# Performance work log

Measured on AMD Instinct MI355X. Metric: run time of the kernel, lower is better.

## Reference

```python
import jax, jax.numpy as jnp
import numpy as np

B, N, M, E = 2, 16384, 16384, 49152
W_CHAMFER, W_EDGE = 1.0, 0.1


def setup_inputs() -> dict:
    key = jax.random.key(0)
    k1, k2, k3 = jax.random.split(key, 3)
    pred_verts = jax.random.normal(k1, (B, N, 3), dtype=jnp.float32)
    target_verts = jax.random.normal(k2, (B, M, 3), dtype=jnp.float32)
    edges = jax.random.randint(k3, (E, 2), 0, N, dtype=jnp.int64)
    return {"pred_verts": pred_verts, "target_verts": target_verts, "edges": edges}


def reference(pred_verts, target_verts, edges):
    # --- Chamfer distance (torch.cdist + bidirectional min) ---
    # Squared-distance expansion avoids materializing the B x N x M x 3 diff tensor.
    p2 = jnp.sum(pred_verts * pred_verts, axis=-1)            # [B, N]
    t2 = jnp.sum(target_verts * target_verts, axis=-1)        # [B, M]
    cross = jnp.einsum('bnd,bmd->bnm', pred_verts, target_verts)  # [B, N, M]
    d2 = p2[:, :, None] + t2[:, None, :] - 2.0 * cross
    dist = jnp.sqrt(jnp.maximum(d2, 0.0))                     # [B, N, M]
    c_loss = jnp.mean(jnp.min(dist, axis=2)) + jnp.mean(jnp.min(dist, axis=1))

    # --- Edge-length variance regularization (vectorized over batch) ---
    v1 = pred_verts[:, edges[:, 0]]                           # [B, E, 3]
    v2 = pred_verts[:, edges[:, 1]]                           # [B, E, 3]
    edge_lengths = jnp.linalg.norm(v1 - v2, axis=-1)          # [B, E]
    # torch.var defaults to unbiased (ddof=1); mean over batch == sum/B
    e_loss = jnp.mean(jnp.var(edge_lengths, axis=1, ddof=1))

    total_loss = W_CHAMFER * c_loss + W_EDGE * e_loss
    return (total_loss, c_loss, e_loss)
```

## Files before the change

kernel.cpp:

```cpp
#include <hip/hip_runtime.h>
#include <float.h>

#define B_SZ 2
#define N_SZ 16384
#define E_SZ 49152

#define TPB 512
#define WAVES (TPB / 64)
#define ROWS_PER_BLOCK 128
#define CHUNK 1024
#define NCHUNK (N_SZ / CHUNK)
#define TILES_PER_CHUNK (CHUNK / 32)
#define TILES_PER_CG (TILES_PER_CHUNK / 4)

#define CH_BLOCKS_PER_DIR (B_SZ * N_SZ / ROWS_PER_BLOCK)
#define CH_BLOCKS (2 * CH_BLOCKS_PER_DIR)
#define EDGE_BLOCKS (B_SZ * E_SZ / TPB)

#define PLANE_BYTES (N_SZ * 16)
#define BATCH_FRAG_BYTES (2 * PLANE_BYTES)
#define DIR_FRAG_BYTES (B_SZ * BATCH_FRAG_BYTES)
#define SUMS_OFF (2 * DIR_FRAG_BYTES)

typedef short short8 __attribute__((ext_vector_type(8)));
typedef float f32x16 __attribute__((ext_vector_type(16)));

__device__ inline short f2bf(float f) {
    unsigned u = __float_as_uint(f);
    unsigned r = (u + 0x7fffu + ((u >> 16) & 1u)) >> 16;
    return (short)r;
}
__device__ inline float bf2f(short s) {
    return __uint_as_float(((unsigned)(unsigned short)s) << 16);
}

typedef __attribute__((address_space(1))) const unsigned int g_u32;
typedef __attribute__((address_space(3))) unsigned int l_u32;
__device__ inline void gload_lds16(const void* g, void* l) {
    __builtin_amdgcn_global_load_lds((g_u32*)g, (l_u32*)l, 16, 0, 0);
}

__global__ __launch_bounds__(TPB) void prep(const float* __restrict__ pred,
                                            const float* __restrict__ tgt,
                                            char* __restrict__ ws) {
    int idx = blockIdx.x * TPB + threadIdx.x;
    double* sums = (double*)(ws + SUMS_OFF);
    if (blockIdx.x == 0 && threadIdx.x < 6) sums[threadIdx.x] = 0.0;

    const bool isTgt = idx < B_SZ * N_SZ;
    int row = isTgt ? idx : idx - B_SZ * N_SZ;
    int batch = row >> 14, pt = row & (N_SZ - 1);
    const float* src = (isTgt ? tgt : pred) + (size_t)row * 3;
    char* base = ws + (isTgt ? 0 : DIR_FRAG_BYTES) + (size_t)batch * BATCH_FRAG_BYTES;

    float tx = src[0], ty = src[1], tz = src[2];
    short hx = f2bf(tx), hy = f2bf(ty), hz = f2bf(tz);
    short lx = f2bf(tx - bf2f(hx)), ly = f2bf(ty - bf2f(hy)), lz = f2bf(tz - bf2f(hz));
    float t2 = fmaf(tx, tx, fmaf(ty, ty, tz * tz));
    short t2h = f2bf(t2), t2l = f2bf(t2 - bf2f(t2h));
    const short one = 0x3f80;

    *(short8*)(base + (size_t)pt * 16) = (short8){hx, hy, hz, hx, hy, hz, one, one};
    *(short8*)(base + PLANE_BYTES + (size_t)pt * 16) =
        (short8){lx, ly, lz, t2h, t2l, 0, 0, 0};
}

__global__ __launch_bounds__(TPB, 4) void main_kernel(
    const float* __restrict__ pred, const float* __restrict__ tgt,
    const int* __restrict__ edges, char* __restrict__ ws)
{
    __shared__ __align__(16) char sB[2][2 * CHUNK * 16];
    __shared__ float wred[WAVES], wred2[WAVES];
    __shared__ int rowMin[ROWS_PER_BLOCK];
    double* sums = (double*)(ws + SUMS_OFF);
    const int lane = threadIdx.x & 63;
    const int wv = threadIdx.x >> 6;
    const int t = threadIdx.x;

    if (blockIdx.x < CH_BLOCKS) {
        const int dir = blockIdx.x >> 8;
        const int xb = blockIdx.x & 255;
        const int batch = xb >> 7;
        const int rowInB = (xb & 127) * ROWS_PER_BLOCK;
        const float* P = dir ? tgt : pred;
        const char* fragBase = ws + (size_t)dir * DIR_FRAG_BYTES
                                  + (size_t)batch * BATCH_FRAG_BYTES;
        const int bl = lane & 31;
        const int half = lane >> 5;
        const int rp = wv & 1;
        const int cg = wv >> 1;

        auto stage = [&](int c, int buf) {
            const char* p0 = fragBase + (size_t)c * (CHUNK * 16);
            const char* p1 = fragBase + PLANE_BYTES + (size_t)c * (CHUNK * 16);
            char* d = sB[buf];
            gload_lds16(p0 + (size_t)t * 16,         d + (size_t)t * 16);
            gload_lds16(p0 + (size_t)(t + TPB) * 16, d + (size_t)(t + TPB) * 16);
            gload_lds16(p1 + (size_t)t * 16,         d + (size_t)(t + 2 * TPB) * 16);
            gload_lds16(p1 + (size_t)(t + TPB) * 16, d + (size_t)(t + 3 * TPB) * 16);
        };
        stage(0, 0);
        if (t < ROWS_PER_BLOCK) rowMin[t] = 0x7f7fffff;

        const short one = 0x3f80;
        short8 af[2];
        #pragma unroll
        for (int j = 0; j < 2; j++) {
            int r = batch * N_SZ + rowInB + rp * 64 + j * 32 + bl;
            const float* p = P + (size_t)r * 3;
            float px = p[0], py = p[1], pz = p[2];
            float ax = -2.f * px, ay = -2.f * py, az = -2.f * pz;
            short ahx = f2bf(ax), ahy = f2bf(ay), ahz = f2bf(az);
            short alx = f2bf(ax - bf2f(ahx)), aly = f2bf(ay - bf2f(ahy)),
                  alz = f2bf(az - bf2f(ahz));
            float p2 = fmaf(px, px, fmaf(py, py, pz * pz));
            short p2h = f2bf(p2), p2l = f2bf(p2 - bf2f(p2h));
            af[j] = half == 0
                ? (short8){ahx, ahy, ahz, alx, aly, alz, p2h, p2l}
                : (short8){ahx, ahy, ahz, one, one, 0, 0, 0};
        }

        float acc0[16], acc1[16];
        #pragma unroll
        for (int e = 0; e < 16; e++) { acc0[e] = FLT_MAX; acc1[e] = FLT_MAX; }
        const f32x16 zc = {0.f, 0.f, 0.f, 0.f, 0.f, 0.f, 0.f, 0.f,
                           0.f, 0.f, 0.f, 0.f, 0.f, 0.f, 0.f, 0.f};

        __syncthreads();

        for (int c = 0; c < NCHUNK; c++) {
            int buf = c & 1;
            if (c + 1 < NCHUNK) stage(c + 1, buf ^ 1);
            const char* bp = sB[buf] + half * (CHUNK * 16)
                           + (size_t)(cg * TILES_PER_CG * 32 + bl) * 16;
            #pragma unroll 1
            for (int mt = 0; mt < TILES_PER_CG; mt += 2) {
                short8 b0 = *(const short8*)(bp + (mt * 32) * 16);
                short8 b1 = *(const short8*)(bp + (mt * 32 + 32) * 16);
                {
                    f32x16 r0 = __builtin_amdgcn_mfma_f32_32x32x16_bf16(af[0], b0, zc, 0, 0, 0);
                    f32x16 r1 = __builtin_amdgcn_mfma_f32_32x32x16_bf16(af[0], b1, zc, 0, 0, 0);
                    #pragma unroll
                    for (int e = 0; e < 16; e++)
                        acc0[e] = fminf(fminf(r0[e], r1[e]), acc0[e]);
                }
                {
                    f32x16 r0 = __builtin_amdgcn_mfma_f32_32x32x16_bf16(af[1], b0, zc, 0, 0, 0);
                    f32x16 r1 = __builtin_amdgcn_mfma_f32_32x32x16_bf16(af[1], b1, zc, 0, 0, 0);
                    #pragma unroll
                    for (int e = 0; e < 16; e++)
                        acc1[e] = fminf(fminf(r0[e], r1[e]), acc1[e]);
                }
            }
            __syncthreads();
        }

        #pragma unroll
        for (int j = 0; j < 2; j++) {
            #pragma unroll
            for (int e = 0; e < 16; e++) {
                float v = (j == 0) ? acc0[e] : acc1[e];
                v = fminf(v, __shfl_xor(v, 1));
                v = fminf(v, __shfl_xor(v, 2));
                v = fminf(v, __shfl_xor(v, 4));
                v = fminf(v, __shfl_xor(v, 8));
                v = fminf(v, __shfl_xor(v, 16));
                if (bl == 0) {
                    int row = rp * 64 + j * 32 + (e & 3) + 8 * (e >> 2) + 4 * half;
                    atomicMin(&rowMin[row], __float_as_int(fmaxf(v, 0.f)));
                }
            }
        }
        __syncthreads();

        if (t < ROWS_PER_BLOCK) {
            float s = sqrtf(__int_as_float(rowMin[t]));
            #pragma unroll
            for (int o = 32; o > 0; o >>= 1) s += __shfl_down(s, o, 64);
            if (lane == 0) wred[wv] = s;
        }
        __syncthreads();
        if (t == 0) atomicAdd(&sums[dir], (double)(wred[0] + wred[1]));
    } else {
        int idx = (blockIdx.x - CH_BLOCKS) * TPB + threadIdx.x;
        int b = idx >= E_SZ;
        int e = idx - b * E_SZ;
        int2 ee = ((const int2*)edges)[e];
        const float* p0 = pred + ((size_t)b * N_SZ + (size_t)ee.x) * 3;
        const float* p1 = pred + ((size_t)b * N_SZ + (size_t)ee.y) * 3;
        float dx = p0[0] - p1[0], dy = p0[1] - p1[1], dz = p0[2] - p1[2];
        float len = sqrtf(dx * dx + dy * dy + dz * dz);
        float s = len, q = len * len;
        for (int o = 32; o > 0; o >>= 1) {
            s += __shfl_down(s, o, 64);
            q += __shfl_down(q, o, 64);
        }
        if (lane == 0) { wred[wv] = s; wred2[wv] = q; }
        __syncthreads();
        if (threadIdx.x == 0) {
            float ts = 0.f, tq = 0.f;
            #pragma unroll
            for (int w = 0; w < WAVES; w++) { ts += wred[w]; tq += wred2[w]; }
            atomicAdd(&sums[2 + 2 * b], (double)ts);
            atomicAdd(&sums[3 + 2 * b], (double)tq);
        }
    }
}

__global__ void final_kernel(const char* __restrict__ ws, float* __restrict__ out) {
    const double* sums = (const double*)(ws + SUMS_OFF);
    double c = sums[0] / (double)(B_SZ * N_SZ) + sums[1] / (double)(B_SZ * N_SZ);
    double e = 0.0;
    #pragma unroll
    for (int b = 0; b < B_SZ; b++) {
        double s = sums[2 + 2 * b], q = sums[3 + 2 * b];
        e += (q - s * s / (double)E_SZ) / (double)(E_SZ - 1);
    }
    e *= (1.0 / B_SZ);
    double tot = 1.0 * c + 0.1 * e;
    out[0] = (float)tot;
    out[1] = (float)c;
    out[2] = (float)e;
}

extern "C" void kernel_launch(void* const* d_in, const int* in_sizes, int n_in,
                              void* d_out, int out_size, void* d_ws, size_t ws_size,
                              hipStream_t stream) {
    const float* pred = (const float*)d_in[0];
    const float* tgt  = (const float*)d_in[1];
    const int* edges  = (const int*)d_in[2];
    float* out = (float*)d_out;
    char* ws = (char*)d_ws;

    prep<<<dim3((2 * B_SZ * N_SZ) / TPB), TPB, 0, stream>>>(pred, tgt, ws);

    main_kernel<<<dim3(CH_BLOCKS + EDGE_BLOCKS), TPB, 0, stream>>>(
        pred, tgt, edges, ws);

    final_kernel<<<dim3(1), dim3(1), 0, stream>>>(ws, out);
}
```

Measured before the change: 103.5 us.

## Fuse prep, chamfer, edge and final stages into one cooperative kernel

Replaces three kernel launches with a single cooperative kernel of 256 blocks that runs prep, a grid sync, the edge and chamfer stages, another grid sync, and the final reduction. Each block now handles both chamfer directions in sequence instead of one block per direction. Edge sums go straight to global double atomics per wave instead of a block reduction, and the inner tile loop is fully unrolled. This removes launch gaps and the tail kernel, at the cost of grid-wide sync overhead, half as many resident blocks, more double atomics, and less parallelism for overlapping the chamfer work.

```diff
diff --git a/kernel.cpp b/kernel.cpp
--- a/kernel.cpp
+++ b/kernel.cpp
@@ -1,22 +1,23 @@
 #include <hip/hip_runtime.h>
+#include <hip/hip_cooperative_groups.h>
 #include <float.h>
+
+namespace cg = cooperative_groups;
 
 #define B_SZ 2
 #define N_SZ 16384
 #define E_SZ 49152
 
+#define GRID 256
 #define TPB 512
 #define WAVES (TPB / 64)
+#define REPS 2
 #define ROWS_PER_BLOCK 128
 #define CHUNK 1024
 #define NCHUNK (N_SZ / CHUNK)
 #define TILES_PER_CHUNK (CHUNK / 32)
 #define TILES_PER_CG (TILES_PER_CHUNK / 4)
 
-#define CH_BLOCKS_PER_DIR (B_SZ * N_SZ / ROWS_PER_BLOCK)
-#define CH_BLOCKS (2 * CH_BLOCKS_PER_DIR)
-#define EDGE_BLOCKS (B_SZ * E_SZ / TPB)
-
 #define PLANE_BYTES (N_SZ * 16)
 #define BATCH_FRAG_BYTES (2 * PLANE_BYTES)
 #define DIR_FRAG_BYTES (B_SZ * BATCH_FRAG_BYTES)
@@ -40,55 +41,75 @@
     __builtin_amdgcn_global_load_lds((g_u32*)g, (l_u32*)l, 16, 0, 0);
 }
 
-__global__ __launch_bounds__(TPB) void prep(const float* __restrict__ pred,
-                                            const float* __restrict__ tgt,
-                                            char* __restrict__ ws) {
-    int idx = blockIdx.x * TPB + threadIdx.x;
-    double* sums = (double*)(ws + SUMS_OFF);
-    if (blockIdx.x == 0 && threadIdx.x < 6) sums[threadIdx.x] = 0.0;
-
-    const bool isTgt = idx < B_SZ * N_SZ;
-    int row = isTgt ? idx : idx - B_SZ * N_SZ;
-    int batch = row >> 14, pt = row & (N_SZ - 1);
-    const float* src = (isTgt ? tgt : pred) + (size_t)row * 3;
-    char* base = ws + (isTgt ? 0 : DIR_FRAG_BYTES) + (size_t)batch * BATCH_FRAG_BYTES;
-
-    float tx = src[0], ty = src[1], tz = src[2];
-    short hx = f2bf(tx), hy = f2bf(ty), hz = f2bf(tz);
-    short lx = f2bf(tx - bf2f(hx)), ly = f2bf(ty - bf2f(hy)), lz = f2bf(tz - bf2f(hz));
-    float t2 = fmaf(tx, tx, fmaf(ty, ty, tz * tz));
-    short t2h = f2bf(t2), t2l = f2bf(t2 - bf2f(t2h));
-    const short one = 0x3f80;
-
-    *(short8*)(base + (size_t)pt * 16) = (short8){hx, hy, hz, hx, hy, hz, one, one};
-    *(short8*)(base + PLANE_BYTES + (size_t)pt * 16) =
-        (short8){lx, ly, lz, t2h, t2l, 0, 0, 0};
-}
-
-__global__ __launch_bounds__(TPB, 4) void main_kernel(
+__global__ __launch_bounds__(TPB, 2) void mega(
     const float* __restrict__ pred, const float* __restrict__ tgt,
-    const int* __restrict__ edges, char* __restrict__ ws)
+    const int* __restrict__ edges, char* __restrict__ ws,
+    float* __restrict__ out)
 {
     __shared__ __align__(16) char sB[2][2 * CHUNK * 16];
-    __shared__ float wred[WAVES], wred2[WAVES];
+    __shared__ float wred[WAVES];
     __shared__ int rowMin[ROWS_PER_BLOCK];
     double* sums = (double*)(ws + SUMS_OFF);
     const int lane = threadIdx.x & 63;
     const int wv = threadIdx.x >> 6;
     const int t = threadIdx.x;
-
-    if (blockIdx.x < CH_BLOCKS) {
-        const int dir = blockIdx.x >> 8;
-        const int xb = blockIdx.x & 255;
-        const int batch = xb >> 7;
-        const int rowInB = (xb & 127) * ROWS_PER_BLOCK;
+    const int gid = blockIdx.x * TPB + threadIdx.x;
+    cg::grid_group grid = cg::this_grid();
+
+    if (gid < 6) sums[gid] = 0.0;
+    if (gid < 2 * B_SZ * N_SZ) {
+        const bool isTgt = gid < B_SZ * N_SZ;
+        int row = isTgt ? gid : gid - B_SZ * N_SZ;
+        int batch = row >> 14, pt = row & (N_SZ - 1);
+        const float* src = (isTgt ? tgt : pred) + (size_t)row * 3;
+        char* base = ws + (isTgt ? 0 : DIR_FRAG_BYTES)
+                        + (size_t)batch * BATCH_FRAG_BYTES;
+        float tx = src[0], ty = src[1], tz = src[2];
+        short hx = f2bf(tx), hy = f2bf(ty), hz = f2bf(tz);
+        short lx = f2bf(tx - bf2f(hx)), ly = f2bf(ty - bf2f(hy)),
+              lz = f2bf(tz - bf2f(hz));
+        float t2 = fmaf(tx, tx, fmaf(ty, ty, tz * tz));
+        short t2h = f2bf(t2), t2l = f2bf(t2 - bf2f(t2h));
+        const short onep = 0x3f80;
+        *(short8*)(base + (size_t)pt * 16) =
+            (short8){hx, hy, hz, hx, hy, hz, onep, onep};
+        *(short8*)(base + PLANE_BYTES + (size_t)pt * 16) =
+            (short8){lx, ly, lz, t2h, t2l, 0, 0, 0};
+    }
+    grid.sync();
+
+    if (gid < 2 * E_SZ) {
+        int b = gid >= E_SZ;
+        int e = gid - b * E_SZ;
+        int2 ee = ((const int2*)edges)[e];
+        const float* p0 = pred + ((size_t)b * N_SZ + (size_t)ee.x) * 3;
+        const float* p1 = pred + ((size_t)b * N_SZ + (size_t)ee.y) * 3;
+        float dx = p0[0] - p1[0], dy = p0[1] - p1[1], dz = p0[2] - p1[2];
+        float len = sqrtf(dx * dx + dy * dy + dz * dz);
+        float s = len, q = len * len;
+        for (int o = 32; o > 0; o >>= 1) {
+            s += __shfl_down(s, o, 64);
+            q += __shfl_down(q, o, 64);
+        }
+        if (lane == 0) {
+            atomicAdd(&sums[2 + 2 * b], (double)s);
+            atomicAdd(&sums[3 + 2 * b], (double)q);
+        }
+    }
+
+    const int bl = lane & 31;
+    const int half = lane >> 5;
+    const int rp = wv & 1;
+    const int cg_ = wv >> 1;
+    const int batch = blockIdx.x >> 7;
+    const int rowInB = (blockIdx.x & 127) * ROWS_PER_BLOCK;
+    const short one = 0x3f80;
+
+    for (int rep = 0; rep < REPS; rep++) {
+        const int dir = rep;
         const float* P = dir ? tgt : pred;
         const char* fragBase = ws + (size_t)dir * DIR_FRAG_BYTES
                                   + (size_t)batch * BATCH_FRAG_BYTES;
-        const int bl = lane & 31;
-        const int half = lane >> 5;
-        const int rp = wv & 1;
-        const int cg = wv >> 1;
 
         auto stage = [&](int c, int buf) {
             const char* p0 = fragBase + (size_t)c * (CHUNK * 16);
@@ -102,7 +123,6 @@
         stage(0, 0);
         if (t < ROWS_PER_BLOCK) rowMin[t] = 0x7f7fffff;
 
-        const short one = 0x3f80;
         short8 af[2];
         #pragma unroll
         for (int j = 0; j < 2; j++) {
@@ -132,8 +152,8 @@
             int buf = c & 1;
             if (c + 1 < NCHUNK) stage(c + 1, buf ^ 1);
             const char* bp = sB[buf] + half * (CHUNK * 16)
-                           + (size_t)(cg * TILES_PER_CG * 32 + bl) * 16;
-            #pragma unroll 1
+                           + (size_t)(cg_ * TILES_PER_CG * 32 + bl) * 16;
+            #pragma unroll
             for (int mt = 0; mt < TILES_PER_CG; mt += 2) {
                 short8 b0 = *(const short8*)(bp + (mt * 32) * 16);
                 short8 b1 = *(const short8*)(bp + (mt * 32 + 32) * 16);
@@ -181,46 +201,23 @@
         }
         __syncthreads();
         if (t == 0) atomicAdd(&sums[dir], (double)(wred[0] + wred[1]));
-    } else {
-        int idx = (blockIdx.x - CH_BLOCKS) * TPB + threadIdx.x;
-        int b = idx >= E_SZ;
-        int e = idx - b * E_SZ;
-        int2 ee = ((const int2*)edges)[e];
-        const float* p0 = pred + ((size_t)b * N_SZ + (size_t)ee.x) * 3;
-        const float* p1 = pred + ((size_t)b * N_SZ + (size_t)ee.y) * 3;
-        float dx = p0[0] - p1[0], dy = p0[1] - p1[1], dz = p0[2] - p1[2];
-        float len = sqrtf(dx * dx + dy * dy + dz * dz);
-        float s = len, q = len * len;
-        for (int o = 32; o > 0; o >>= 1) {
-            s += __shfl_down(s, o, 64);
-            q += __shfl_down(q, o, 64);
-        }
-        if (lane == 0) { wred[wv] = s; wred2[wv] = q; }
-        __syncthreads();
-        if (threadIdx.x == 0) {
-            float ts = 0.f, tq = 0.f;
-            #pragma unroll
-            for (int w = 0; w < WAVES; w++) { ts += wred[w]; tq += wred2[w]; }
-            atomicAdd(&sums[2 + 2 * b], (double)ts);
-            atomicAdd(&sums[3 + 2 * b], (double)tq);
-        }
-    }
-}
-
-__global__ void final_kernel(const char* __restrict__ ws, float* __restrict__ out) {
-    const double* sums = (const double*)(ws + SUMS_OFF);
-    double c = sums[0] / (double)(B_SZ * N_SZ) + sums[1] / (double)(B_SZ * N_SZ);
-    double e = 0.0;
-    #pragma unroll
-    for (int b = 0; b < B_SZ; b++) {
-        double s = sums[2 + 2 * b], q = sums[3 + 2 * b];
-        e += (q - s * s / (double)E_SZ) / (double)(E_SZ - 1);
-    }
-    e *= (1.0 / B_SZ);
-    double tot = 1.0 * c + 0.1 * e;
-    out[0] = (float)tot;
-    out[1] = (float)c;
-    out[2] = (float)e;
+    }
+
+    grid.sync();
+    if (blockIdx.x == 0 && threadIdx.x == 0) {
+        double c = sums[0] / (double)(B_SZ * N_SZ) + sums[1] / (double)(B_SZ * N_SZ);
+        double e = 0.0;
+        #pragma unroll
+        for (int b = 0; b < B_SZ; b++) {
+            double s = sums[2 + 2 * b], q = sums[3 + 2 * b];
+            e += (q - s * s / (double)E_SZ) / (double)(E_SZ - 1);
+        }
+        e *= (1.0 / B_SZ);
+        double tot = 1.0 * c + 0.1 * e;
+        out[0] = (float)tot;
+        out[1] = (float)c;
+        out[2] = (float)e;
+    }
 }
 
 extern "C" void kernel_launch(void* const* d_in, const int* in_sizes, int n_in,
@@ -232,10 +229,6 @@
     float* out = (float*)d_out;
     char* ws = (char*)d_ws;
 
-    prep<<<dim3((2 * B_SZ * N_SZ) / TPB), TPB, 0, stream>>>(pred, tgt, ws);
-
-    main_kernel<<<dim3(CH_BLOCKS + EDGE_BLOCKS), TPB, 0, stream>>>(
-        pred, tgt, edges, ws);
-
-    final_kernel<<<dim3(1), dim3(1), 0, stream>>>(ws, out);
-}
+    void* args[] = {(void*)&pred, (void*)&tgt, (void*)&edges, (void*)&ws, (void*)&out};
+    hipLaunchCooperativeKernel((void*)mega, dim3(GRID), dim3(TPB), args, 0, stream);
+}
```

Result: slower. 244.6 us (+136.3%).

## Replace LDS double-buffered staging with direct global register prefetch of B fragments

Applied to the files above, without the earlier changes.

Removes the shared-memory chunk staging (global_load_lds double buffer plus per-chunk barriers) and has each wave load its B-operand fragments straight from global memory into registers, prefetching the next four tiles while the MFMAs run on the current ones. Each column group now walks a contiguous quarter of all tiles instead of a slice of each chunk. The launch-bounds occupancy hint drops from 4 to 2 blocks per CU to give more registers for the prefetched fragments. This removes LDS traffic and barrier stalls but relies on L2/L1 caching, since every block rereads the whole fragment array from global memory, and lower occupancy may expose latency.

```diff
diff --git a/kernel.cpp b/kernel.cpp
--- a/kernel.cpp
+++ b/kernel.cpp
@@ -8,10 +8,8 @@
 #define TPB 512
 #define WAVES (TPB / 64)
 #define ROWS_PER_BLOCK 128
-#define CHUNK 1024
-#define NCHUNK (N_SZ / CHUNK)
-#define TILES_PER_CHUNK (CHUNK / 32)
-#define TILES_PER_CG (TILES_PER_CHUNK / 4)
+#define NTILES (N_SZ / 32)
+#define TILES_PER_CG (NTILES / 4)
 
 #define CH_BLOCKS_PER_DIR (B_SZ * N_SZ / ROWS_PER_BLOCK)
 #define CH_BLOCKS (2 * CH_BLOCKS_PER_DIR)
@@ -32,12 +30,6 @@
 }
 __device__ inline float bf2f(short s) {
     return __uint_as_float(((unsigned)(unsigned short)s) << 16);
-}
-
-typedef __attribute__((address_space(1))) const unsigned int g_u32;
-typedef __attribute__((address_space(3))) unsigned int l_u32;
-__device__ inline void gload_lds16(const void* g, void* l) {
-    __builtin_amdgcn_global_load_lds((g_u32*)g, (l_u32*)l, 16, 0, 0);
 }
 
 __global__ __launch_bounds__(TPB) void prep(const float* __restrict__ pred,
@@ -65,11 +57,10 @@
         (short8){lx, ly, lz, t2h, t2l, 0, 0, 0};
 }
 
-__global__ __launch_bounds__(TPB, 4) void main_kernel(
+__global__ __launch_bounds__(TPB, 2) void main_kernel(
     const float* __restrict__ pred, const float* __restrict__ tgt,
     const int* __restrict__ edges, char* __restrict__ ws)
 {
-    __shared__ __align__(16) char sB[2][2 * CHUNK * 16];
     __shared__ float wred[WAVES], wred2[WAVES];
     __shared__ int rowMin[ROWS_PER_BLOCK];
     double* sums = (double*)(ws + SUMS_OFF);
@@ -90,16 +81,6 @@
         const int rp = wv & 1;
         const int cg = wv >> 1;
 
-        auto stage = [&](int c, int buf) {
-            const char* p0 = fragBase + (size_t)c * (CHUNK * 16);
-            const char* p1 = fragBase + PLANE_BYTES + (size_t)c * (CHUNK * 16);
-            char* d = sB[buf];
-            gload_lds16(p0 + (size_t)t * 16,         d + (size_t)t * 16);
-            gload_lds16(p0 + (size_t)(t + TPB) * 16, d + (size_t)(t + TPB) * 16);
-            gload_lds16(p1 + (size_t)t * 16,         d + (size_t)(t + 2 * TPB) * 16);
-            gload_lds16(p1 + (size_t)(t + TPB) * 16, d + (size_t)(t + 3 * TPB) * 16);
-        };
-        stage(0, 0);
         if (t < ROWS_PER_BLOCK) rowMin[t] = 0x7f7fffff;
 
         const short one = 0x3f80;
@@ -126,33 +107,44 @@
         const f32x16 zc = {0.f, 0.f, 0.f, 0.f, 0.f, 0.f, 0.f, 0.f,
                            0.f, 0.f, 0.f, 0.f, 0.f, 0.f, 0.f, 0.f};
 
-        __syncthreads();
-
-        for (int c = 0; c < NCHUNK; c++) {
-            int buf = c & 1;
-            if (c + 1 < NCHUNK) stage(c + 1, buf ^ 1);
-            const char* bp = sB[buf] + half * (CHUNK * 16)
-                           + (size_t)(cg * TILES_PER_CG * 32 + bl) * 16;
-            #pragma unroll 1
-            for (int mt = 0; mt < TILES_PER_CG; mt += 2) {
-                short8 b0 = *(const short8*)(bp + (mt * 32) * 16);
-                short8 b1 = *(const short8*)(bp + (mt * 32 + 32) * 16);
-                {
-                    f32x16 r0 = __builtin_amdgcn_mfma_f32_32x32x16_bf16(af[0], b0, zc, 0, 0, 0);
-                    f32x16 r1 = __builtin_amdgcn_mfma_f32_32x32x16_bf16(af[0], b1, zc, 0, 0, 0);
-                    #pragma unroll
-                    for (int e = 0; e < 16; e++)
-                        acc0[e] = fminf(fminf(r0[e], r1[e]), acc0[e]);
-                }
-                {
-                    f32x16 r0 = __builtin_amdgcn_mfma_f32_32x32x16_bf16(af[1], b0, zc, 0, 0, 0);
-                    f32x16 r1 = __builtin_amdgcn_mfma_f32_32x32x16_bf16(af[1], b1, zc, 0, 0, 0);
-                    #pragma unroll
-                    for (int e = 0; e < 16; e++)
-                        acc1[e] = fminf(fminf(r0[e], r1[e]), acc1[e]);
-                }
+        const char* bbase = fragBase + (size_t)half * PLANE_BYTES
+                                     + (size_t)bl * 16;
+        const int tbase = cg * TILES_PER_CG;
+        auto ldb = [&](int tc) {
+            return *(const short8*)(bbase + (size_t)tc * 512);
+        };
+
+        #define DOPAIR(X0, X1)                                                 \
+            do {                                                               \
+                f32x16 r0 = __builtin_amdgcn_mfma_f32_32x32x16_bf16(af[0], X0, zc, 0, 0, 0); \
+                f32x16 r1 = __builtin_amdgcn_mfma_f32_32x32x16_bf16(af[0], X1, zc, 0, 0, 0); \
+                _Pragma("unroll")                                              \
+                for (int e = 0; e < 16; e++)                                   \
+                    acc0[e] = fminf(fminf(r0[e], r1[e]), acc0[e]);             \
+                f32x16 s0 = __builtin_amdgcn_mfma_f32_32x32x16_bf16(af[1], X0, zc, 0, 0, 0); \
+                f32x16 s1 = __builtin_amdgcn_mfma_f32_32x32x16_bf16(af[1], X1, zc, 0, 0, 0); \
+                _Pragma("unroll")                                              \
+                for (int e = 0; e < 16; e++)                                   \
+                    acc1[e] = fminf(fminf(s0[e], s1[e]), acc1[e]);             \
+            } while (0)
+
+        short8 b0 = ldb(tbase + 0), b1 = ldb(tbase + 1);
+        short8 b2 = ldb(tbase + 2), b3 = ldb(tbase + 3);
+        __syncthreads();
+
+        #pragma unroll 1
+        for (int i = 0; i < TILES_PER_CG / 4; i++) {
+            int pf = (i < TILES_PER_CG / 4 - 1) ? tbase + 4 * (i + 1) : tbase;
+            {
+                short8 x0 = b0, x1 = b1;
+                b0 = ldb(pf + 0); b1 = ldb(pf + 1);
+                DOPAIR(x0, x1);
             }
-            __syncthreads();
+            {
+                short8 x0 = b2, x1 = b3;
+                b2 = ldb(pf + 2); b3 = ldb(pf + 3);
+                DOPAIR(x0, x1);
+            }
         }
 
         #pragma unroll
```

New measurement: 104.0 us. No clear change (+0.5%).
